# Kernel optimization log

Hardware: AMD Instinct MI355X
Metric: run time of the kernel (lower is better)

Reference implementation:

```python
import jax, jax.numpy as jnp
import numpy as np

EMB = 2048
N_HEADS = 16
HEAD_DIM = 128
N_KV = 4
ROPE_BASE = 10000.0
B, S = 2, 2048


def _rope(x, cos, sin):
    # x: [B,S,h,d]; cos/sin: [1,S,1,d//2]
    x1, x2 = x[..., ::2], x[..., 1::2]
    return jnp.concatenate([x1 * cos - x2 * sin, x1 * sin + x2 * cos], axis=-1)


def setup_inputs() -> dict:
    key = jax.random.key(0)
    ks = jax.random.split(key, 5)
    x = jax.random.normal(ks[0], (B, S, EMB), dtype=jnp.float32)
    wq = jax.random.normal(ks[1], (EMB, N_HEADS * HEAD_DIM), dtype=jnp.float32) * 0.02
    wk = jax.random.normal(ks[2], (EMB, N_KV * HEAD_DIM), dtype=jnp.float32) * 0.02
    wv = jax.random.normal(ks[3], (EMB, N_KV * HEAD_DIM), dtype=jnp.float32) * 0.02
    wo = jax.random.normal(ks[4], (N_HEADS * HEAD_DIM, EMB), dtype=jnp.float32) * 0.02
    mask = jnp.tril(jnp.ones((S, S), dtype=bool))[None, None]  # [1,1,S,S] causal
    return {"x": x, "wq": wq, "wk": wk, "wv": wv, "wo": wo, "mask": mask}


def reference(x, wq, wk, wv, wo, mask):
    b, s, _ = x.shape
    q = (x @ wq).reshape(b, s, N_HEADS, HEAD_DIM)
    k = (x @ wk).reshape(b, s, N_KV, HEAD_DIM)
    v = (x @ wv).reshape(b, s, N_KV, HEAD_DIM)

    pos = jnp.arange(s, dtype=jnp.float32)
    dim_range = jnp.arange(0, HEAD_DIM, 2, dtype=jnp.float32)
    freqs = 1.0 / ROPE_BASE ** (dim_range / HEAD_DIM)
    angles = pos[:, None] * freqs[None, :]            # [S, d/2]
    cos = jnp.cos(angles)[None, :, None, :]           # [1,S,1,d/2]
    sin = jnp.sin(angles)[None, :, None, :]

    q = _rope(q, cos, sin)
    k = _rope(k, cos, sin)

    rep = N_HEADS // N_KV
    k = jnp.tile(k, (1, 1, rep, 1))  # matches torch .repeat on group dim
    v = jnp.tile(v, (1, 1, rep, 1))

    scale = 1.0 / jnp.sqrt(jnp.float32(HEAD_DIM))
    scores = jnp.einsum('bqhd,bkhd->bhqk', q, k) * scale  # [B,H,S,S]
    scores = jnp.where(mask, scores, -jnp.inf)
    attn = jax.nn.softmax(scores, axis=-1)  # dropout is identity in eval
    out = jnp.einsum('bhqk,bkhd->bqhd', attn, v).reshape(b, s, N_HEADS * HEAD_DIM)
    return out @ wo
```

## Files before the change

kernel.cpp:

```cpp
#include <hip/hip_runtime.h>

#define EMB 2048
#define NH 16
#define NKV 4
#define HD 128
#define SLEN 2048
#define BSZ 2
#define MROWS (BSZ * SLEN)

#define QOFF (BSZ * NH * SLEN * HD)
#define KOFF (BSZ * NKV * SLEN * HD)

typedef __attribute__((ext_vector_type(8))) short bf16x8;
typedef __attribute__((ext_vector_type(4))) float f32x4;
typedef __attribute__((ext_vector_type(2))) float f32x2;
typedef __attribute__((ext_vector_type(4))) short s16x4;

__device__ __forceinline__ short f2bf(float f) {
  union { float f; unsigned u; } v; v.f = f;
  unsigned r = (v.u + 0x7fffu + ((v.u >> 16) & 1u)) >> 16;
  return (short)r;
}

__global__ void rope_tab_k(f32x2* __restrict__ tab) {
  int i = blockIdx.x * blockDim.x + threadIdx.x;
  if (i >= SLEN * 64) return;
  int s = i >> 6, j = i & 63;
  float freq = exp2f(-(float)j * (13.287712379549449f / 64.0f));
  float ang = (float)s * freq;
  float sv, cv;
  sincosf(ang, &sv, &cv);
  f32x2 cs; cs[0] = cv; cs[1] = sv;
  tab[i] = cs;
}

__global__ void cast_bf16_k(const float* __restrict__ in, short* __restrict__ outp, int n) {
  int i = (blockIdx.x * blockDim.x + threadIdx.x) * 4;
  if (i >= n) return;
  f32x4 v = *(const f32x4*)(in + i);
  s16x4 r;
#pragma unroll
  for (int k = 0; k < 4; ++k) r[k] = f2bf(v[k]);
  *(s16x4*)(outp + i) = r;
}

__global__ void transpose_cast_k(const float* __restrict__ in, short* __restrict__ outp,
                                 int R, int C) {
  __shared__ float t[32][33];
  int c0 = blockIdx.x * 32, r0 = blockIdx.y * 32;
  int tx = threadIdx.x, ty = threadIdx.y;
#pragma unroll
  for (int i = 0; i < 4; ++i)
    t[ty + i * 8][tx] = in[(size_t)(r0 + ty + i * 8) * C + (c0 + tx)];
  __syncthreads();
#pragma unroll
  for (int i = 0; i < 4; ++i)
    outp[(size_t)(c0 + ty + i * 8) * R + (r0 + tx)] = f2bf(t[tx][ty + i * 8]);
}

#define GLL16(g, l)                                                        \
  __builtin_amdgcn_global_load_lds(                                        \
      (const __attribute__((address_space(1))) void*)(g),                  \
      (__attribute__((address_space(3))) void*)(l), 16, 0, 0)

template <int EPI>
__global__ __launch_bounds__(256, 2) void gemm_bt_k(
    const short* __restrict__ A, const short* __restrict__ Bt,
    float* __restrict__ Cf, short* __restrict__ Cb,
    int M, int N, int K, const f32x2* __restrict__ rope) {
  __shared__ short lA[3][128 * 32];
  __shared__ short lB[3][128 * 32];
  int tid = threadIdx.x;
  int lane = tid & 63, wid = tid >> 6;
  int m0 = blockIdx.y * 128, n0 = blockIdx.x * 128;
  int wr = (wid >> 1) * 64, wc = (wid & 1) * 64;
  int l16 = lane & 15, lk4 = lane >> 4;
  const int K2B = K * 2;
  const char* Ab = (const char*)A;
  const char* Bb = (const char*)Bt;
  (void)M;

  auto stage = [&](int slot, int k0) {
#pragma unroll
    for (int r = 0; r < 2; ++r) {
      int X = tid * 16 + r * 4096;
      int row = X >> 6, cb = X & 63;
      int logical = cb ^ ((row & 3) << 4);
      GLL16(Ab + (size_t)(m0 + row) * K2B + k0 * 2 + logical, (char*)&lA[slot][0] + X);
      GLL16(Bb + (size_t)(n0 + row) * K2B + k0 * 2 + logical, (char*)&lB[slot][0] + X);
    }
  };
  auto ldA = [&](int slot, int m) {
    int row = wr + m * 16 + l16;
    return *(const bf16x8*)((char*)&lA[slot][0] + row * 64 + ((lk4 * 16) ^ ((row & 3) << 4)));
  };
  auto ldB = [&](int slot, int n) {
    int row = wc + n * 16 + l16;
    return *(const bf16x8*)((char*)&lB[slot][0] + row * 64 + ((lk4 * 16) ^ ((row & 3) << 4)));
  };

  f32x4 acc[4][4] = {};
  stage(0, 0);
  stage(1, 32);
  int nk = K / 32;
  for (int t = 0; t < nk; ++t) {
    int slot = t % 3;
    if (t + 1 < nk) asm volatile("s_waitcnt vmcnt(4)" ::: "memory");
    else            asm volatile("s_waitcnt vmcnt(0)" ::: "memory");
    __builtin_amdgcn_s_barrier();
    __builtin_amdgcn_sched_barrier(0);
    bf16x8 af[4], bfv[4];
#pragma unroll
    for (int m = 0; m < 4; ++m) af[m] = ldA(slot, m);
#pragma unroll
    for (int n = 0; n < 4; ++n) bfv[n] = ldB(slot, n);
    __builtin_amdgcn_s_setprio(1);
#pragma unroll
    for (int m = 0; m < 4; ++m)
#pragma unroll
      for (int n = 0; n < 4; ++n)
        acc[m][n] = __builtin_amdgcn_mfma_f32_16x16x32_bf16(af[m], bfv[n], acc[m][n], 0, 0, 0);
    __builtin_amdgcn_s_setprio(0);
    if (t + 2 < nk) stage((t + 2) % 3, (t + 2) * 32);
  }

  const float SCL2E = 0.08838834764831845f * 1.4426950408889634f;
#pragma unroll
  for (int m = 0; m < 4; ++m) {
#pragma unroll
    for (int n = 0; n < 4; ++n) {
#pragma unroll
      for (int j = 0; j < 4; ++j) {
        int gm = m0 + wr + m * 16 + lk4 * 4 + j;
        int gc = n0 + wc + n * 16 + l16;
        float v = acc[m][n][j];
        if constexpr (EPI == 0) {
          Cf[(size_t)gm * N + gc] = v;
        } else {
          int pos = gm & (SLEN - 1), bb = gm >> 11;
          if (gc < 2560) {
            float p = __shfl_xor(v, 1);
            bool isq = gc < 2048;
            int gcc = isq ? gc : gc - 2048;
            int head = gcc >> 7, d = gcc & 127;
            f32x2 cs = rope[pos * 64 + (d >> 1)];
            float ov = ((d & 1) == 0) ? (v * cs[0] - p * cs[1])
                                      : (p * cs[1] + v * cs[0]);
            if (isq) ov *= SCL2E;
            size_t idx = isq
                ? (((size_t)(bb * NH + head) * SLEN + pos) * HD + d)
                : ((size_t)QOFF + ((size_t)(bb * NKV + head) * SLEN + pos) * HD + d);
            Cb[idx] = f2bf(ov);
          } else {
            int gcc = gc - 2560;
            int head = gcc >> 7, d = gcc & 127;
            Cb[(size_t)QOFF + KOFF + ((size_t)(bb * NKV + head) * HD + d) * SLEN + pos] = f2bf(v);
          }
        }
      }
    }
  }
}

__global__ __launch_bounds__(512, 2) void flash_k(
    const short* __restrict__ Qb, const short* __restrict__ Kb,
    const short* __restrict__ Vt, short* __restrict__ O) {
  __shared__ short lK[4][64 * 128];
  __shared__ short lV[4][128 * 64];
  __shared__ short Plds[8][16][64];

  int tid = threadIdx.x, lane = tid & 63, wid = tid >> 6;
  int bh = blockIdx.y;
  int b = bh >> 4, h = bh & 15, kv = h & 3;
  int l16 = lane & 15, lk4 = lane >> 4;
  int qtA = 15 - (int)blockIdx.x;
  int qtB = (int)blockIdx.x;
  int ntA = 2 * (qtA + 1);
  int ntot = ntA + 2 * (qtB + 1);

  const short* qptr = Qb + (size_t)(b * NH + h) * SLEN * HD;
  const char* kg = (const char*)(Kb + (size_t)(b * NKV + kv) * SLEN * HD);
  const char* vg = (const char*)(Vt + (size_t)(b * NKV + kv) * HD * SLEN);

  int qbw = qtA * 128 + wid * 16;
  bf16x8 aq[4];
#pragma unroll
  for (int c = 0; c < 4; ++c)
    aq[c] = *(const bf16x8*)(qptr + (size_t)(qbw + l16) * HD + c * 32 + lk4 * 8);

  f32x4 o[8] = {};
  float m = -__builtin_inff();
  float lsum = 0.0f;

  char* myP = (char*)&Plds[wid][0][0];
  int swz = (l16 & 7) << 4;
  int swzk = l16 << 4;

  auto stageKV = [&](int buf, int k0) {
#pragma unroll
    for (int r = 0; r < 2; ++r) {
      int X = tid * 16 + r * 8192;
      int row = X >> 8, cb = X & 255;
      GLL16(kg + (size_t)(k0 + row) * 256 + (cb ^ ((row & 15) << 4)),
            (char*)&lK[buf][0] + X);
    }
#pragma unroll
    for (int r = 0; r < 2; ++r) {
      int X = tid * 16 + r * 8192;
      int row = X >> 7, cb = X & 127;
      GLL16(vg + (size_t)row * (SLEN * 2) + k0 * 2 + (cb ^ ((row & 7) << 4)),
            (char*)&lV[buf][0] + X);
    }
  };
  auto k0_of = [&](int t) { return (t < ntA ? t : t - ntA) * 64; };

  auto finalize = [&]() {
    float ls = lsum;
    ls += __shfl_xor(ls, 16);
    ls += __shfl_xor(ls, 32);
    float inv = 1.0f / ls;
    size_t ro = ((size_t)(b * SLEN + qbw + l16)) * (NH * HD) + h * HD;
#pragma unroll
    for (int dt = 0; dt < 8; ++dt) {
      s16x4 r;
#pragma unroll
      for (int j = 0; j < 4; ++j) r[j] = f2bf(o[dt][j] * inv);
      *(s16x4*)(O + ro + dt * 16 + lk4 * 4) = r;
    }
  };

  stageKV(0, k0_of(0));
  stageKV(1, k0_of(1));
  stageKV(2, k0_of(2));

  for (int tt = 0; tt < ntot; ++tt) {
    int rem = ntot - 1 - tt;
    if (rem >= 2)      asm volatile("s_waitcnt vmcnt(8)" ::: "memory");
    else if (rem == 1) asm volatile("s_waitcnt vmcnt(4)" ::: "memory");
    else               asm volatile("s_waitcnt vmcnt(0)" ::: "memory");
    __builtin_amdgcn_s_barrier();
    __builtin_amdgcn_sched_barrier(0);

    if (tt == ntA) {
      finalize();
#pragma unroll
      for (int dt = 0; dt < 8; ++dt) o[dt] = (f32x4){0.f, 0.f, 0.f, 0.f};
      m = -__builtin_inff();
      lsum = 0.0f;
      qbw = qtB * 128 + wid * 16;
#pragma unroll
      for (int c = 0; c < 4; ++c)
        aq[c] = *(const bf16x8*)(qptr + (size_t)(qbw + l16) * HD + c * 32 + lk4 * 8);
    }

    int k0 = k0_of(tt);
    int buf = tt & 3;
    if (k0 < qbw + 16) {
      const char* Kbase = (const char*)&lK[buf][0];
      const char* Vbase = (const char*)&lV[buf][0];
      f32x4 s[4] = {};
      __builtin_amdgcn_s_setprio(1);
#pragma unroll
      for (int c = 0; c < 4; ++c) {
#pragma unroll
        for (int t = 0; t < 4; ++t) {
          bf16x8 bk = *(const bf16x8*)(Kbase + (t * 16 + l16) * 256 + ((c * 64 + lk4 * 16) ^ swzk));
          s[t] = __builtin_amdgcn_mfma_f32_16x16x32_bf16(bk, aq[c], s[t], 0, 0, 0);
        }
      }
      __builtin_amdgcn_s_setprio(0);
      float x[16];
#pragma unroll
      for (int t = 0; t < 4; ++t)
#pragma unroll
        for (int j = 0; j < 4; ++j) x[t * 4 + j] = s[t][j];
      if (k0 + 63 > qbw) {
        int kq = k0 + lk4 * 4 - qbw - l16;
#pragma unroll
        for (int t = 0; t < 4; ++t)
#pragma unroll
          for (int j = 0; j < 4; ++j)
            if (kq + t * 16 + j > 0) x[t * 4 + j] = -3.0e38f;
      }
      float a0 = fmaxf(x[0], x[1]), a1 = fmaxf(x[2], x[3]);
      float a2 = fmaxf(x[4], x[5]), a3 = fmaxf(x[6], x[7]);
      float a4 = fmaxf(x[8], x[9]), a5 = fmaxf(x[10], x[11]);
      float a6 = fmaxf(x[12], x[13]), a7 = fmaxf(x[14], x[15]);
      float b0 = fmaxf(fmaxf(a0, a1), fmaxf(a2, a3));
      float b1 = fmaxf(fmaxf(a4, a5), fmaxf(a6, a7));
      float tm = fmaxf(b0, b1);
      tm = fmaxf(tm, __shfl_xor(tm, 16));
      tm = fmaxf(tm, __shfl_xor(tm, 32));
      float mn = fmaxf(m, tm);
      if (!__all(tm <= m + 8.0f)) {
        float f = __builtin_amdgcn_exp2f(m - mn);
        m = mn;
        lsum *= f;
#pragma unroll
        for (int dt = 0; dt < 8; ++dt) o[dt] *= f;
      }
      float psum = 0.0f;
#pragma unroll
      for (int t = 0; t < 4; ++t) {
        float p0 = __builtin_amdgcn_exp2f(x[t * 4 + 0] - m);
        float p1 = __builtin_amdgcn_exp2f(x[t * 4 + 1] - m);
        float p2 = __builtin_amdgcn_exp2f(x[t * 4 + 2] - m);
        float p3 = __builtin_amdgcn_exp2f(x[t * 4 + 3] - m);
        psum += (p0 + p1) + (p2 + p3);
        unsigned lo, hi;
        asm("v_cvt_pk_bf16_f32 %0, %1, %2" : "=v"(lo) : "v"(p0), "v"(p1));
        asm("v_cvt_pk_bf16_f32 %0, %1, %2" : "=v"(hi) : "v"(p2), "v"(p3));
        unsigned long long dw = ((unsigned long long)hi << 32) | lo;
        *(unsigned long long*)(myP + ((l16 * 128 + t * 32 + lk4 * 8) ^ swz)) = dw;
      }
      lsum += psum;
      asm volatile("s_waitcnt lgkmcnt(0)" ::: "memory");
      __builtin_amdgcn_sched_barrier(0);
      __builtin_amdgcn_s_setprio(1);
#pragma unroll
      for (int hh = 0; hh < 2; ++hh) {
        bf16x8 pa = *(const bf16x8*)(myP + ((l16 * 128 + hh * 64 + lk4 * 16) ^ swz));
#pragma unroll
        for (int dt = 0; dt < 8; ++dt) {
          bf16x8 bv = *(const bf16x8*)(Vbase + (dt * 16 + l16) * 128 + ((hh * 64 + lk4 * 16) ^ swz));
          o[dt] = __builtin_amdgcn_mfma_f32_16x16x32_bf16(bv, pa, o[dt], 0, 0, 0);
        }
      }
      __builtin_amdgcn_s_setprio(0);
    }
    if (tt + 3 < ntot) stageKV((tt + 3) & 3, k0_of(tt + 3));
  }
  finalize();
}

extern "C" void kernel_launch(void* const* d_in, const int* in_sizes, int n_in,
                              void* d_out, int out_size, void* d_ws, size_t ws_size,
                              hipStream_t stream) {
  const float* x  = (const float*)d_in[0];
  const float* wq = (const float*)d_in[1];
  const float* wk = (const float*)d_in[2];
  const float* wv = (const float*)d_in[3];
  const float* wo = (const float*)d_in[4];
  float* out = (float*)d_out;
  char* ws = (char*)d_ws;
  (void)in_sizes; (void)n_in; (void)out_size; (void)ws_size;

  const size_t MB = 1024 * 1024;
  f32x2* rope   = (f32x2*)(ws);
  short* xb     = (short*)(ws + 1 * MB);
  short* wqkvT  = (short*)(ws + 17 * MB);
  short* woT    = (short*)(ws + 29 * MB);
  short* QKVb   = (short*)(ws + 37 * MB);
  short* O      = xb;

  short* Qb = QKVb;
  short* Kb = QKVb + QOFF;
  short* Vt = QKVb + QOFF + KOFF;

  rope_tab_k<<<(SLEN * 64 + 255) / 256, 256, 0, stream>>>(rope);
  cast_bf16_k<<<(MROWS * EMB / 4 + 255) / 256, 256, 0, stream>>>(x, xb, MROWS * EMB);

  dim3 tb(32, 8);
  transpose_cast_k<<<dim3(2048 / 32, 2048 / 32), tb, 0, stream>>>(wq, wqkvT, 2048, 2048);
  transpose_cast_k<<<dim3(512 / 32, 2048 / 32), tb, 0, stream>>>(wk, wqkvT + 2048 * 2048, 2048, 512);
  transpose_cast_k<<<dim3(512 / 32, 2048 / 32), tb, 0, stream>>>(wv, wqkvT + 2560 * 2048, 2048, 512);
  transpose_cast_k<<<dim3(2048 / 32, 2048 / 32), tb, 0, stream>>>(wo, woT, 2048, 2048);

  gemm_bt_k<5><<<dim3(3072 / 128, MROWS / 128), 256, 0, stream>>>(xb, wqkvT, nullptr, QKVb, MROWS, 3072, 2048, rope);

  flash_k<<<dim3(8, BSZ * NH), 512, 0, stream>>>(Qb, Kb, Vt, O);

  gemm_bt_k<0><<<dim3(2048 / 128, MROWS / 128), 256, 0, stream>>>(O, woT, out, nullptr, MROWS, 2048, 2048, rope);
}
```

Measured before the change: 211.2 us.

## Give each wave private LDS staging buffers and drop block barriers in GEMM

The GEMM's shared 128x32 A/B tiles are replaced with per-wave private LDS buffers (double-buffered), where each wave loads its own 64-row slices of A and B. This removes the block-wide s_barrier from the k-loop, and the next stage is issued right after fragments are read into registers. In exchange, each A and B row slice is now loaded twice across waves (waves sharing rows duplicate global traffic), and LDS use rises to 64KB per block, which may limit occupancy to one block per CU.

```diff
diff --git a/kernel.cpp b/kernel.cpp
--- a/kernel.cpp
+++ b/kernel.cpp
@@ -68,8 +68,7 @@
     const short* __restrict__ A, const short* __restrict__ Bt,
     float* __restrict__ Cf, short* __restrict__ Cb,
     int M, int N, int K, const f32x2* __restrict__ rope) {
-  __shared__ short lA[3][128 * 32];
-  __shared__ short lB[3][128 * 32];
+  __shared__ char Lds[4][2][8192];
   int tid = threadIdx.x;
   int lane = tid & 63, wid = tid >> 6;
   int m0 = blockIdx.y * 128, n0 = blockIdx.x * 128;
@@ -78,25 +77,28 @@
   const int K2B = K * 2;
   const char* Ab = (const char*)A;
   const char* Bb = (const char*)Bt;
+  char (*Lw)[8192] = Lds[wid];
   (void)M;
 
   auto stage = [&](int slot, int k0) {
-#pragma unroll
-    for (int r = 0; r < 2; ++r) {
-      int X = tid * 16 + r * 4096;
+    char* la = &Lw[slot][0];
+    char* lb = &Lw[slot][4096];
+#pragma unroll
+    for (int i = 0; i < 4; ++i) {
+      int X = lane * 16 + i * 1024;
       int row = X >> 6, cb = X & 63;
       int logical = cb ^ ((row & 3) << 4);
-      GLL16(Ab + (size_t)(m0 + row) * K2B + k0 * 2 + logical, (char*)&lA[slot][0] + X);
-      GLL16(Bb + (size_t)(n0 + row) * K2B + k0 * 2 + logical, (char*)&lB[slot][0] + X);
+      GLL16(Ab + (size_t)(m0 + wr + row) * K2B + k0 * 2 + logical, la + X);
+      GLL16(Bb + (size_t)(n0 + wc + row) * K2B + k0 * 2 + logical, lb + X);
     }
   };
   auto ldA = [&](int slot, int m) {
-    int row = wr + m * 16 + l16;
-    return *(const bf16x8*)((char*)&lA[slot][0] + row * 64 + ((lk4 * 16) ^ ((row & 3) << 4)));
+    int r = m * 16 + l16;
+    return *(const bf16x8*)(&Lw[slot][0] + r * 64 + ((lk4 * 16) ^ ((r & 3) << 4)));
   };
   auto ldB = [&](int slot, int n) {
-    int row = wc + n * 16 + l16;
-    return *(const bf16x8*)((char*)&lB[slot][0] + row * 64 + ((lk4 * 16) ^ ((row & 3) << 4)));
+    int r = n * 16 + l16;
+    return *(const bf16x8*)(&Lw[slot][4096] + r * 64 + ((lk4 * 16) ^ ((r & 3) << 4)));
   };
 
   f32x4 acc[4][4] = {};
@@ -104,16 +106,19 @@
   stage(1, 32);
   int nk = K / 32;
   for (int t = 0; t < nk; ++t) {
-    int slot = t % 3;
-    if (t + 1 < nk) asm volatile("s_waitcnt vmcnt(4)" ::: "memory");
+    int slot = t & 1;
+    if (t + 1 < nk) asm volatile("s_waitcnt vmcnt(8)" ::: "memory");
     else            asm volatile("s_waitcnt vmcnt(0)" ::: "memory");
-    __builtin_amdgcn_s_barrier();
     __builtin_amdgcn_sched_barrier(0);
     bf16x8 af[4], bfv[4];
 #pragma unroll
     for (int m = 0; m < 4; ++m) af[m] = ldA(slot, m);
 #pragma unroll
     for (int n = 0; n < 4; ++n) bfv[n] = ldB(slot, n);
+    asm volatile("s_waitcnt lgkmcnt(0)" ::: "memory");
+    __builtin_amdgcn_sched_barrier(0);
+    if (t + 2 < nk) stage(slot, (t + 2) * 32);
+    __builtin_amdgcn_sched_barrier(0);
     __builtin_amdgcn_s_setprio(1);
 #pragma unroll
     for (int m = 0; m < 4; ++m)
@@ -121,7 +126,6 @@
       for (int n = 0; n < 4; ++n)
         acc[m][n] = __builtin_amdgcn_mfma_f32_16x16x32_bf16(af[m], bfv[n], acc[m][n], 0, 0, 0);
     __builtin_amdgcn_s_setprio(0);
-    if (t + 2 < nk) stage((t + 2) % 3, (t + 2) * 32);
   }
 
   const float SCL2E = 0.08838834764831845f * 1.4426950408889634f;
```

After: 256.7 us. +21.5%, slower.
